# Optimization experiments

Hardware: AMD Instinct MI355X
Metric: run time of the kernel (lower is better)

The kernel has to match this reference:

```python
import jax, jax.numpy as jnp
import numpy as np


def setup_inputs() -> dict:
    key = jax.random.key(0)
    k1, k2, k3, k4, k5, k6 = jax.random.split(key, 6)
    B, V = 128, 128000
    logits = jax.random.normal(k1, (B, V), dtype=jnp.float32) * 2.0
    # keep temperatures away from 0 to avoid overflow in logits/temp
    temperatures = 0.7 + 0.6 * jax.random.uniform(k2, (B,), dtype=jnp.float32)
    top_ks = jax.random.randint(k3, (B,), 1, 1024, dtype=jnp.int32)
    top_ps = 0.7 + 0.29 * jax.random.uniform(k4, (B,), dtype=jnp.float32)
    min_ps = 0.02 * jax.random.uniform(k5, (B,), dtype=jnp.float32)
    # uniform variate for inverse-CDF multinomial sampling (one sample per row)
    u = jax.random.uniform(k6, (B, 1), dtype=jnp.float32)
    return {
        "logits": logits,
        "temperatures": temperatures,
        "top_ks": top_ks,
        "top_ps": top_ps,
        "min_ps": min_ps,
        "u": u,
    }


def reference(logits, temperatures, top_ks, top_ps, min_ps, u):
    """Faithful jax version of Sampler's torch-native sampling path:
    softmax(logits/T) -> descending sort -> top-k mask -> top-p mask
    (cumsum computed pre-mask, exactly as torch code) -> min-p mask ->
    multinomial sample (inverse CDF with provided uniform u) ->
    gather original token index. Also returns the renormalized filtered
    probs scattered back to vocab order (top_p_normalize_probs-style)."""
    B, V = logits.shape
    probs = jax.nn.softmax(logits / temperatures[:, None], axis=-1)  # [B, V]

    order = jnp.argsort(-probs, axis=-1)                     # descending indices
    probs_sort = jnp.take_along_axis(probs, order, axis=-1)  # [B, V] sorted desc
    probs_sum = jnp.cumsum(probs_sort, axis=-1)              # cumsum BEFORE masking

    pos = jnp.arange(V, dtype=jnp.int32)[None, :]
    # top-k: zero everything at rank >= top_k
    probs_sort = jnp.where(pos >= top_ks[:, None], 0.0, probs_sort)
    # top-p: zero where cumulative mass strictly before this token exceeds top_p
    probs_sort = jnp.where(probs_sum - probs_sort > top_ps[:, None], 0.0, probs_sort)
    # min-p: threshold relative to the max prob (rank-0 entry survives both masks)
    min_p_thr = probs_sort[:, :1] * min_ps[:, None]
    probs_sort = jnp.where(probs_sort < min_p_thr, 0.0, probs_sort)

    total = jnp.sum(probs_sort, axis=-1, keepdims=True)      # [B, 1]
    cdf = jnp.cumsum(probs_sort, axis=-1) / total            # normalized CDF
    # inverse-CDF sampling == torch.multinomial(probs_sort, 1)
    sampled_rank = jnp.clip(jnp.sum(cdf < u, axis=-1, keepdims=True), 0, V - 1)
    token_ids = jnp.take_along_axis(order, sampled_rank, axis=-1)[:, 0].astype(jnp.int32)

    # scatter renormalized filtered probs back to original vocab positions
    inv_order = jnp.argsort(order, axis=-1)
    norm_probs = jnp.take_along_axis(probs_sort / total, inv_order, axis=-1)
    return token_ids, norm_probs
```

## Files before the change

kernel.cpp:

```cpp
#include <hip/hip_runtime.h>
#include <stdint.h>
#include <math.h>

#define TPB 1024
#define NB 2048
#define SPLIT 4
#define LCAND 2560
#define CAND2 2048
#define PS 4096
#define L2E 1.44269504088896f

typedef float vfloat4 __attribute__((ext_vector_type(4)));
typedef unsigned long long ull;

__device__ __forceinline__ unsigned fkey(float f) {
    unsigned u = __float_as_uint(f);
    return (u & 0x80000000u) ? ~u : (u | 0x80000000u);
}
__device__ __forceinline__ float funkey(unsigned k) {
    unsigned u = (k & 0x80000000u) ? (k ^ 0x80000000u) : ~k;
    return __uint_as_float(u);
}
__device__ __forceinline__ ull packkv(unsigned k, unsigned idx) {
    return ((ull)k << 32) | (ull)(~idx);
}

__device__ __forceinline__ void suffix_scan_2048(unsigned* h, unsigned* wscr, int tid)
{
    const int lane = tid & 63, w = tid >> 6;
    const int i0 = 2047 - 2 * tid;
    const int i1 = 2046 - 2 * tid;
    unsigned a = h[i0], b = h[i1];
    unsigned s = a + b;
    unsigned inc = s;
    #pragma unroll
    for (int d = 1; d < 64; d <<= 1) { unsigned o = __shfl_up(inc, d); if (lane >= d) inc += o; }
    if (lane == 63) wscr[w] = inc;
    __syncthreads();
    if (w == 0) {
        unsigned v = (lane < 16) ? wscr[lane] : 0u;
        unsigned vi = v;
        #pragma unroll
        for (int d = 1; d < 16; d <<= 1) { unsigned o = __shfl_up(vi, d); if (lane >= d) vi += o; }
        if (lane < 16) wscr[16 + lane] = vi - v;
    }
    __syncthreads();
    unsigned off = wscr[16 + w] + (inc - s);
    h[i0] = off + a;
    h[i1] = off + a + b;
    __syncthreads();
}

__global__ __launch_bounds__(TPB)
void k1_scan(const float* __restrict__ logits,
             const float* __restrict__ temps,
             const int* __restrict__ top_ks,
             float* __restrict__ out_probs,
             float* __restrict__ ws_meta,
             unsigned* __restrict__ ws_cut,
             unsigned* __restrict__ ws_cnt,
             ull* __restrict__ ws_cand,
             int V, int Vq)
{
    const int sblk = blockIdx.x;
    const int b = sblk / SPLIT, s = sblk % SPLIT;
    const int tid = threadIdx.x, lane = tid & 63, w = tid >> 6;
    const int start = s * Vq;
    const int len = min(Vq, V - start);
    const int slot = sblk;
    const float invT = 1.0f / temps[b];
    int K = top_ks[b]; K = max(K, 1); K = min(K, 1024);

    __shared__ unsigned hist[NB];
    __shared__ unsigned uscr[32];
    __shared__ float fred[32];
    __shared__ unsigned cnt;
    __shared__ int bstar;

    if (len <= 0) {
        if (tid == 0) {
            ws_meta[2*slot] = -1e30f; ws_meta[2*slot+1] = 0.0f;
            ws_cut[slot] = 0xFFFFFFFFu; ws_cnt[slot] = 0u;
        }
        return;
    }

    for (int i = tid; i < NB; i += TPB) hist[i] = 0;
    if (tid == 0) { cnt = 0; bstar = 0; }
    __syncthreads();

    const float* __restrict__ row = logits + (size_t)b * V + start;
    const vfloat4* __restrict__ row4 = (const vfloat4*)row;
    const int L4 = len >> 2;

    const int nps = min(len, PS);
    float m0 = -1e30f;
    for (int i = tid; i < nps; i += TPB) {
        float lv = row[i];
        m0 = fmaxf(m0, lv);
        atomicAdd(&hist[fkey(lv) >> 21], 1u);
    }
    #pragma unroll
    for (int d = 32; d > 0; d >>= 1) m0 = fmaxf(m0, __shfl_down(m0, d));
    if (lane == 0) fred[w] = m0;
    __syncthreads();
    if (tid == 0) {
        float mm = fred[0];
        for (int j = 1; j < 16; ++j) mm = fmaxf(mm, fred[j]);
        fred[16] = mm;
    }
    __syncthreads();
    const float m0max = fred[16];

    suffix_scan_2048(hist, uscr, tid);
    float sexp = (float)K * (float)nps / (float)V;
    unsigned TGT = (unsigned)(sexp + 6.0f * sqrtf(sexp) + 16.5f);
    if (TGT > (unsigned)nps) TGT = (unsigned)nps;
    for (int e = tid; e < NB; e += TPB) {
        unsigned Se = hist[e];
        unsigned Sn = (e < NB - 1) ? hist[e + 1] : 0u;
        if (Se >= TGT && Sn < TGT) bstar = e;
    }
    __syncthreads();
    const unsigned cutkey = (unsigned)bstar << 21;
    const float cutval = funkey(cutkey);

    {
        float* __restrict__ orow = out_probs + (size_t)b * V + start;
        vfloat4* __restrict__ orow4 = (vfloat4*)orow;
        const vfloat4 z4 = (vfloat4)0.0f;
        for (int i = tid; i < L4; i += TPB) __builtin_nontemporal_store(z4, &orow4[i]);
        for (int i = (L4 << 2) + tid; i < len; i += TPB) __builtin_nontemporal_store(0.0f, &orow[i]);
    }

    const float ca = invT * L2E;
    const float cb = -m0max * invT * L2E;
    ull* gc = ws_cand + (size_t)slot * LCAND;

    float z0 = 0.0f, z1 = 0.0f, z2 = 0.0f, z3 = 0.0f;

    #define E4(v) (exp2f(fmaf((v)[0], ca, cb)) + exp2f(fmaf((v)[1], ca, cb)) \
                 + exp2f(fmaf((v)[2], ca, cb)) + exp2f(fmaf((v)[3], ca, cb)))
    #define GATHER(v, ii) do {                                                  \
        bool c0 = (v)[0] >= cutval, c1 = (v)[1] >= cutval,                      \
             c2 = (v)[2] >= cutval, c3 = (v)[3] >= cutval;                      \
        if (c0 | c1 | c2 | c3) {                                                \
            int nh = (int)c0 + (int)c1 + (int)c2 + (int)c3;                     \
            unsigned base = atomicAdd(&cnt, (unsigned)nh);                      \
            unsigned bi = (unsigned)(start + ((ii) << 2));                      \
            if (c0) { if (base < LCAND) gc[base] = packkv(fkey((v)[0]), bi+0); base++; } \
            if (c1) { if (base < LCAND) gc[base] = packkv(fkey((v)[1]), bi+1); base++; } \
            if (c2) { if (base < LCAND) gc[base] = packkv(fkey((v)[2]), bi+2); base++; } \
            if (c3) { if (base < LCAND) gc[base] = packkv(fkey((v)[3]), bi+3); base++; } \
        }                                                                       \
    } while (0)

    int i = tid;
    for (; i + 3 * TPB < L4; i += 4 * TPB) {
        vfloat4 va = row4[i];
        vfloat4 vb = row4[i + TPB];
        vfloat4 vc = row4[i + 2 * TPB];
        vfloat4 vd = row4[i + 3 * TPB];
        z0 += E4(va); z1 += E4(vb); z2 += E4(vc); z3 += E4(vd);
        GATHER(va, i); GATHER(vb, i + TPB); GATHER(vc, i + 2 * TPB); GATHER(vd, i + 3 * TPB);
    }
    for (; i < L4; i += TPB) {
        vfloat4 v = row4[i];
        z0 += E4(v);
        GATHER(v, i);
    }
    for (int j = (L4 << 2) + tid; j < len; j += TPB) {
        float lv = row[j];
        z0 += exp2f(fmaf(lv, ca, cb));
        if (lv >= cutval) {
            unsigned base = atomicAdd(&cnt, 1u);
            if (base < LCAND) gc[base] = packkv(fkey(lv), (unsigned)(start + j));
        }
    }
    #undef E4
    #undef GATHER

    float z = (z0 + z1) + (z2 + z3);
    __syncthreads();
    #pragma unroll
    for (int d = 32; d > 0; d >>= 1) z += __shfl_down(z, d);
    if (lane == 0) fred[w] = z;
    __syncthreads();
    if (tid == 0) {
        float zz = 0.0f;
        for (int j = 0; j < 16; ++j) zz += fred[j];
        ws_meta[2*slot + 0] = m0max * invT;
        ws_meta[2*slot + 1] = zz;
        ws_cut[slot] = cutkey;
        ws_cnt[slot] = cnt;
    }
}

__global__ __launch_bounds__(TPB)
void k2_sample(const float* __restrict__ logits,
               const float* __restrict__ temps,
               const int* __restrict__ top_ks,
               const float* __restrict__ top_ps,
               const float* __restrict__ min_ps,
               const float* __restrict__ uvec,
               const float* __restrict__ ws_meta,
               const unsigned* __restrict__ ws_cut,
               const unsigned* __restrict__ ws_cnt,
               const ull* __restrict__ ws_cand,
               float* __restrict__ out_tok,
               float* __restrict__ out_probs,
               int V)
{
    const int b = blockIdx.x;
    const int tid = threadIdx.x, lane = tid & 63, w = tid >> 6;
    const float invT = 1.0f / temps[b];
    int Korig = top_ks[b]; Korig = max(Korig, 1); Korig = min(Korig, 1024);
    const unsigned Ku = (unsigned)Korig;
    const float top_p = top_ps[b], min_p = min_ps[b], uval = uvec[b];

    __shared__ __align__(16) char smem[53504];
    ull*            cand  = (ull*)(smem);
    ull*            cand2 = (ull*)(smem + 16384);
    unsigned*       hist  = (unsigned*)(smem + 32768);
    unsigned short* cnts  = (unsigned short*)(smem + 41216);
    float*          sh_p  = (float*)(smem + 45312);
    float*          sh_c  = (float*)(smem + 49408);
    __shared__ unsigned uscr[32];
    __shared__ float fws[32];
    __shared__ unsigned scnt, sh_mk;
    __shared__ int sh_i1, sh_i2;
    __shared__ unsigned sh_u1;

    float Cy[SPLIT], zq[SPLIT];
    unsigned cutq[SPLIT], cntq[SPLIT];
    #pragma unroll
    for (int q = 0; q < SPLIT; ++q) {
        int sl = b * SPLIT + q;
        Cy[q] = ws_meta[2*sl]; zq[q] = ws_meta[2*sl+1];
        cutq[q] = ws_cut[sl]; cntq[q] = ws_cnt[sl];
    }
    float Y = -1e30f;
    #pragma unroll
    for (int q = 0; q < SPLIT; ++q) if (cntq[q] > 0u) Y = fmaxf(Y, Cy[q]);
    float Z = 0.0f;
    #pragma unroll
    for (int q = 0; q < SPLIT; ++q)
        if (cntq[q] > 0u && zq[q] > 0.0f) Z += zq[q] * exp2f((Cy[q] - Y) * L2E);

    bool fb = false;
    unsigned cutmax = 0, mincut = 0xFFFFFFFFu;
    #pragma unroll
    for (int q = 0; q < SPLIT; ++q) {
        if (cntq[q] > (unsigned)LCAND) fb = true;
        if (cntq[q] > 0u) {
            if (!isfinite(zq[q])) fb = true;
            cutmax = max(cutmax, cutq[q]);
            mincut = min(mincut, cutq[q]);
        }
    }
    if (mincut == 0xFFFFFFFFu || !isfinite(Z) || Z <= 0.0f) fb = true;

    unsigned Tkeyb = 0;
    int count = 0, bstar = 0, shift = 0;
    unsigned base = mincut;

    if (!fb) {
        unsigned mk = 0;
        if (tid == 0) sh_mk = 0;
        for (int i = tid; i <= NB; i += TPB) hist[i] = 0;
        if (tid == 0) { sh_i1 = -1; scnt = 0; }
        __syncthreads();
        #pragma unroll
        for (int q = 0; q < SPLIT; ++q) {
            const ull* gc = ws_cand + (size_t)(b * SPLIT + q) * LCAND;
            int nl = min((int)cntq[q], LCAND);
            for (int i = tid; i < nl; i += TPB)
                mk = max(mk, (unsigned)(gc[i] >> 32));
        }
        #pragma unroll
        for (int d = 32; d > 0; d >>= 1) mk = max(mk, __shfl_down(mk, d));
        if (lane == 0) atomicMax(&sh_mk, mk);
        __syncthreads();
        const unsigned maxkey = sh_mk;
        const unsigned range = maxkey - base;
        while ((range >> shift) > (unsigned)(NB - 1)) shift++;

        #pragma unroll
        for (int q = 0; q < SPLIT; ++q) {
            const ull* gc = ws_cand + (size_t)(b * SPLIT + q) * LCAND;
            int nl = min((int)cntq[q], LCAND);
            for (int i = tid; i < nl; i += TPB)
                atomicAdd(&hist[((unsigned)(gc[i] >> 32) - base) >> shift], 1u);
        }
        __syncthreads();
        unsigned fat = 0;
        for (int i = tid; i < NB; i += TPB) {
            unsigned h = hist[i];
            cnts[i] = (unsigned short)h;
            fat = max(fat, h);
        }
        #pragma unroll
        for (int d = 32; d > 0; d >>= 1) fat = max(fat, __shfl_down(fat, d));
        if (lane == 0) uscr[w] = fat;
        __syncthreads();
        if (tid == 0) {
            unsigned m2 = 0;
            for (int j = 0; j < 16; ++j) m2 = max(m2, uscr[j]);
            uscr[16] = m2;
        }
        __syncthreads();
        if (uscr[16] > 64u) fb = true;
    }
    if (!fb) {
        suffix_scan_2048(hist, uscr, tid);
        for (int e = tid; e < NB; e += TPB) {
            unsigned Se = hist[e], Sn = (e < NB - 1) ? hist[e + 1] : 0u;
            if (Se >= Ku && Sn < Ku) { sh_i1 = e; sh_u1 = Se; }
        }
        __syncthreads();
        if (sh_i1 < 0) fb = true;
        else {
            bstar = sh_i1;
            count = (int)sh_u1;
            Tkeyb = base + ((unsigned)bstar << shift);
            if (Tkeyb < cutmax || count > CAND2) fb = true;
        }
    }
    if (!fb) {
        #pragma unroll
        for (int q = 0; q < SPLIT; ++q) {
            const ull* gc = ws_cand + (size_t)(b * SPLIT + q) * LCAND;
            int nl = min((int)cntq[q], LCAND);
            for (int i = tid; i < nl; i += TPB) {
                ull e = gc[i];
                unsigned k = (unsigned)(e >> 32);
                if (k >= Tkeyb) {
                    unsigned bin = (k - base) >> shift;
                    unsigned pos = atomicAdd(&hist[bin + 1], 1u);
                    cand2[pos] = e;
                }
            }
        }
        __syncthreads();
        for (int e = bstar + tid; e < NB; e += TPB) {
            int c = (int)cnts[e];
            if (c >= 2) {
                int st = (int)hist[e + 1] - c;
                for (int x = 1; x < c; ++x) {
                    ull key = cand2[st + x];
                    int y = x - 1;
                    while (y >= 0 && cand2[st + y] < key) { cand2[st + y + 1] = cand2[st + y]; --y; }
                    cand2[st + y + 1] = key;
                }
            }
        }
        __syncthreads();
    }

    if (fb) {
        const float* __restrict__ row = logits + (size_t)b * V;
        float m = -1e30f, z = 0.0f;
        for (int i = tid; i < V; i += TPB) {
            float y = row[i] * invT;
            float nm = fmaxf(m, y);
            z = z * exp2f((m - nm) * L2E) + exp2f((y - nm) * L2E);
            m = nm;
        }
        sh_p[tid] = m; sh_c[tid] = z;
        __syncthreads();
        for (int d = TPB >> 1; d > 0; d >>= 1) {
            if (tid < d) {
                float m1 = sh_p[tid], z1 = sh_c[tid];
                float m2 = sh_p[tid + d], z2 = sh_c[tid + d];
                float mm = fmaxf(m1, m2);
                sh_c[tid] = z1 * exp2f((m1 - mm) * L2E) + z2 * exp2f((m2 - mm) * L2E);
                sh_p[tid] = mm;
            }
            __syncthreads();
        }
        Y = sh_p[0]; Z = sh_c[0];
        __syncthreads();
        for (int i = tid; i < NB; i += TPB) hist[i] = 0;
        if (tid == 0) { sh_i1 = 0; sh_i2 = 0; sh_u1 = 0; }
        __syncthreads();
        for (int i = tid; i < V; i += TPB) atomicAdd(&hist[fkey(row[i]) >> 21], 1u);
        __syncthreads();
        suffix_scan_2048(hist, uscr, tid);
        for (int e = tid; e < NB; e += TPB) {
            unsigned Se = hist[e], Sn = (e < NB-1) ? hist[e+1] : 0u;
            if (Se >= Ku && Sn < Ku) { sh_i1 = e; sh_u1 = Sn; }
        }
        __syncthreads();
        int b1 = sh_i1;
        unsigned cab = sh_u1;
        for (int i = tid; i < NB; i += TPB) hist[i] = 0;
        __syncthreads();
        for (int i = tid; i < V; i += TPB) {
            unsigned k = fkey(row[i]);
            if ((int)(k >> 21) == b1) atomicAdd(&hist[(k >> 10) & (NB - 1)], 1u);
        }
        __syncthreads();
        suffix_scan_2048(hist, uscr, tid);
        for (int e = tid; e < NB; e += TPB) {
            unsigned Se = cab + hist[e];
            unsigned Sn = cab + ((e < NB-1) ? hist[e+1] : 0u);
            if (Se >= Ku && Sn < Ku) sh_i2 = e;
        }
        __syncthreads();
        unsigned Tkey = ((unsigned)b1 << 21) | ((unsigned)sh_i2 << 10);
        if (tid == 0) scnt = 0;
        __syncthreads();
        for (int i = tid; i < V; i += TPB) {
            unsigned k = fkey(row[i]);
            if (k >= Tkey) {
                unsigned pos = atomicAdd(&scnt, 1u);
                if (pos < CAND2) cand[pos] = packkv(k, (unsigned)i);
            }
        }
        __syncthreads();
        count = (scnt < (unsigned)CAND2) ? (int)scnt : CAND2;

        int n_sort = 1;
        while (n_sort < count) n_sort <<= 1;
        for (int i = tid; i < n_sort; i += TPB)
            if (i >= count) cand[i] = 0ull;
        __syncthreads();
        for (int kk = 2; kk <= n_sort; kk <<= 1) {
            for (int j = kk >> 1; j > 0; j >>= 1) {
                for (int i = tid; i < n_sort; i += TPB) {
                    int ixj = i ^ j;
                    if (ixj > i) {
                        ull a = cand[i], c = cand[ixj];
                        bool up = (i & kk) == 0;
                        if (up ? (a < c) : (a > c)) { cand[i] = c; cand[ixj] = a; }
                    }
                }
                __syncthreads();
            }
        }
    }

    ull* srt = fb ? cand : cand2;
    int K = min(Korig, count);

    float pv = 0.0f;
    if (tid < K) {
        unsigned k = (unsigned)(srt[tid] >> 32);
        pv = exp2f((funkey(k) * invT - Y) * L2E) / Z;
    }
    float inc = pv;
    #pragma unroll
    for (int d = 1; d < 64; d <<= 1) { float o = __shfl_up(inc, d); if (lane >= d) inc += o; }
    if (lane == 63) fws[w] = inc;
    __syncthreads();
    if (w == 0) {
        float v = (lane < 16) ? fws[lane] : 0.0f;
        float vi = v;
        #pragma unroll
        for (int d = 1; d < 16; d <<= 1) { float o = __shfl_up(vi, d); if (lane >= d) vi += o; }
        if (lane < 16) fws[16 + lane] = vi - v;
    }
    __syncthreads();
    float cum = inc + fws[16 + w];
    sh_p[tid] = pv;
    sh_c[tid] = cum;
    if (tid == 0) sh_i1 = K;
    __syncthreads();

    if (tid < K) {
        float excl = cum - pv;
        if (excl > top_p) atomicMin(&sh_i1, tid);
    }
    __syncthreads();
    int n1 = sh_i1;
    float thr = sh_p[0] * min_p;
    if (tid == 0) sh_i2 = n1;
    __syncthreads();
    if (tid < n1 && sh_p[tid] < thr) atomicMin(&sh_i2, tid);
    __syncthreads();
    int nf = sh_i2;
    float total = sh_c[nf - 1];

    int pred = (tid < nf) && ((sh_c[tid] / total) < uval);
    int rank = __syncthreads_count(pred);
    if (rank > nf - 1) rank = nf - 1;
    if (rank < 0) rank = 0;
    if (tid == 0)
        out_tok[b] = (float)(~(unsigned)(srt[rank] & 0xFFFFFFFFull));

    if (tid < nf) {
        unsigned idx = ~(unsigned)(srt[tid] & 0xFFFFFFFFull);
        out_probs[(size_t)b * V + idx] = sh_p[tid] / total;
    }
}

extern "C" void kernel_launch(void* const* d_in, const int* in_sizes, int n_in,
                              void* d_out, int out_size, void* d_ws, size_t ws_size,
                              hipStream_t stream) {
    const float* logits = (const float*)d_in[0];
    const float* temps  = (const float*)d_in[1];
    const int*   top_ks = (const int*)d_in[2];
    const float* top_ps = (const float*)d_in[3];
    const float* min_ps = (const float*)d_in[4];
    const float* u      = (const float*)d_in[5];
    const int B = in_sizes[1];
    const int V = in_sizes[0] / B;
    float* out_tok   = (float*)d_out;
    float* out_probs = out_tok + B;

    int Vq = (((V + SPLIT - 1) / SPLIT) + 3) & ~3;

    char* ws = (char*)d_ws;
    size_t off = 0;
    auto take = [&](size_t bytes) { char* p = ws + off; off = (off + bytes + 255) & ~(size_t)255; return p; };
    float*    ws_meta = (float*)take((size_t)B * SPLIT * 2 * sizeof(float));
    unsigned* ws_cut  = (unsigned*)take((size_t)B * SPLIT * sizeof(unsigned));
    unsigned* ws_cnt  = (unsigned*)take((size_t)B * SPLIT * sizeof(unsigned));
    ull*      ws_cand = (ull*)take((size_t)B * SPLIT * LCAND * sizeof(ull));
    (void)ws_size;

    k1_scan<<<dim3(SPLIT * B), dim3(TPB), 0, stream>>>(
        logits, temps, top_ks, out_probs, ws_meta, ws_cut, ws_cnt, ws_cand, V, Vq);
    k2_sample<<<dim3(B), dim3(TPB), 0, stream>>>(
        logits, temps, top_ks, top_ps, min_ps, u, ws_meta, ws_cut, ws_cnt, ws_cand,
        out_tok, out_probs, V);
}
```

Before: 152.5 us.

## Split cut-threshold estimation into separate kernel, double row split, track candidate max

Moves the per-slice sample histogram, max and cutoff selection into a new lightweight k0_cut kernel (256 threads), so the streaming k1 kernel (now 512 threads) only does the exp-sum and candidate gather. The vocabulary split doubles from 4 to 8 slices per row, with a smaller per-slice candidate buffer and a smaller sample prefix. k1 now also reports the maximum candidate key, which removes a full pass over candidates in k2. Zeroing of the output now uses regular stores instead of nontemporal ones. This adds a kernel launch and reads the sample prefix twice. The smaller candidate buffers raise the chance of overflow, which sends rows down the fallback path.

Result: slower. 157.4 us (+3.2%).

```diff
diff --git a/kernel.cpp b/kernel.cpp
--- a/kernel.cpp
+++ b/kernel.cpp
@@ -2,12 +2,14 @@
 #include <stdint.h>
 #include <math.h>
 
+#define T0 256
+#define T1 512
 #define TPB 1024
 #define NB 2048
-#define SPLIT 4
-#define LCAND 2560
+#define SPLIT 8
+#define LCAND 1024
 #define CAND2 2048
-#define PS 4096
+#define PS0 2048
 #define L2E 1.44269504088896f
 
 typedef float vfloat4 __attribute__((ext_vector_type(4)));
@@ -51,93 +53,151 @@
     __syncthreads();
 }
 
-__global__ __launch_bounds__(TPB)
+__global__ __launch_bounds__(T0)
+void k0_cut(const float* __restrict__ logits,
+            const float* __restrict__ temps,
+            const int* __restrict__ top_ks,
+            float* __restrict__ ws_cy,
+            unsigned* __restrict__ ws_cut,
+            int V, int Vq)
+{
+    const int slot = blockIdx.x;
+    const int b = slot / SPLIT, s = slot % SPLIT;
+    const int tid = threadIdx.x, lane = tid & 63, w = tid >> 6;
+    const int start = s * Vq;
+    const int len = min(Vq, V - start);
+
+    __shared__ unsigned hist[NB];
+    __shared__ unsigned uscr[16];
+    __shared__ float fred[8];
+    __shared__ int bstar;
+
+    if (len <= 0) {
+        if (tid == 0) { ws_cut[slot] = 0xFFFFFFFFu; ws_cy[slot] = -1e30f; }
+        return;
+    }
+    for (int i = tid; i < NB; i += T0) hist[i] = 0;
+    if (tid == 0) bstar = 0;
+    __syncthreads();
+
+    const float* __restrict__ row = logits + (size_t)b * V + start;
+    const vfloat4* __restrict__ row4 = (const vfloat4*)row;
+    const int nps = min(len, PS0);
+    const int np4 = nps >> 2;
+
+    float m0 = -1e30f;
+    for (int i = tid; i < np4; i += T0) {
+        vfloat4 v = row4[i];
+        #pragma unroll
+        for (int j = 0; j < 4; ++j) {
+            float lv = v[j];
+            m0 = fmaxf(m0, lv);
+            atomicAdd(&hist[fkey(lv) >> 21], 1u);
+        }
+    }
+    for (int i = (np4 << 2) + tid; i < nps; i += T0) {
+        float lv = row[i];
+        m0 = fmaxf(m0, lv);
+        atomicAdd(&hist[fkey(lv) >> 21], 1u);
+    }
+    #pragma unroll
+    for (int d = 32; d > 0; d >>= 1) m0 = fmaxf(m0, __shfl_down(m0, d));
+    if (lane == 0) fred[w] = m0;
+    __syncthreads();
+    if (tid == 0) {
+        float mm = fred[0];
+        for (int j = 1; j < T0 / 64; ++j) mm = fmaxf(mm, fred[j]);
+        fred[4] = mm;
+    }
+    __syncthreads();
+    const float m0max = fred[4];
+
+    unsigned sloc[8];
+    unsigned acc = 0;
+    #pragma unroll
+    for (int j = 0; j < 8; ++j) { acc += hist[2047 - (8 * tid + j)]; sloc[j] = acc; }
+    __syncthreads();
+    unsigned inc = acc;
+    #pragma unroll
+    for (int d = 1; d < 64; d <<= 1) { unsigned o = __shfl_up(inc, d); if (lane >= d) inc += o; }
+    if (lane == 63) uscr[w] = inc;
+    __syncthreads();
+    if (tid == 0) {
+        unsigned o = 0;
+        for (int j = 0; j < T0 / 64; ++j) { unsigned t = uscr[j]; uscr[8 + j] = o; o += t; }
+    }
+    __syncthreads();
+    unsigned off = uscr[8 + w] + (inc - acc);
+    #pragma unroll
+    for (int j = 0; j < 8; ++j) hist[2047 - (8 * tid + j)] = off + sloc[j];
+    __syncthreads();
+
+    int K = top_ks[b]; K = max(K, 1); K = min(K, 1024);
+    float sexp = (float)K * (float)nps / (float)V;
+    unsigned TGT = (unsigned)(sexp + 6.0f * sqrtf(sexp) + 16.5f);
+    if (TGT > (unsigned)nps) TGT = (unsigned)nps;
+    for (int e = tid; e < NB; e += T0) {
+        unsigned Se = hist[e];
+        unsigned Sn = (e < NB - 1) ? hist[e + 1] : 0u;
+        if (Se >= TGT && Sn < TGT) bstar = e;
+    }
+    __syncthreads();
+    if (tid == 0) {
+        ws_cut[slot] = (unsigned)bstar << 21;
+        ws_cy[slot]  = m0max / temps[b];
+    }
+}
+
+__global__ __launch_bounds__(T1)
 void k1_scan(const float* __restrict__ logits,
              const float* __restrict__ temps,
-             const int* __restrict__ top_ks,
              float* __restrict__ out_probs,
-             float* __restrict__ ws_meta,
-             unsigned* __restrict__ ws_cut,
+             const float* __restrict__ ws_cy,
+             const unsigned* __restrict__ ws_cut,
+             float* __restrict__ ws_z,
              unsigned* __restrict__ ws_cnt,
+             unsigned* __restrict__ ws_maxk,
              ull* __restrict__ ws_cand,
              int V, int Vq)
 {
-    const int sblk = blockIdx.x;
-    const int b = sblk / SPLIT, s = sblk % SPLIT;
+    const int slot = blockIdx.x;
+    const int b = slot / SPLIT, s = slot % SPLIT;
     const int tid = threadIdx.x, lane = tid & 63, w = tid >> 6;
     const int start = s * Vq;
     const int len = min(Vq, V - start);
-    const int slot = sblk;
+
+    __shared__ float fred[16];
+    __shared__ unsigned cnt;
+
+    if (len <= 0) {
+        if (tid == 0) { ws_z[slot] = 0.0f; ws_cnt[slot] = 0u; ws_maxk[slot] = 0u; }
+        return;
+    }
+    if (tid == 0) cnt = 0;
+    __syncthreads();
+
     const float invT = 1.0f / temps[b];
-    int K = top_ks[b]; K = max(K, 1); K = min(K, 1024);
-
-    __shared__ unsigned hist[NB];
-    __shared__ unsigned uscr[32];
-    __shared__ float fred[32];
-    __shared__ unsigned cnt;
-    __shared__ int bstar;
-
-    if (len <= 0) {
-        if (tid == 0) {
-            ws_meta[2*slot] = -1e30f; ws_meta[2*slot+1] = 0.0f;
-            ws_cut[slot] = 0xFFFFFFFFu; ws_cnt[slot] = 0u;
-        }
-        return;
-    }
-
-    for (int i = tid; i < NB; i += TPB) hist[i] = 0;
-    if (tid == 0) { cnt = 0; bstar = 0; }
-    __syncthreads();
+    const float Cy = ws_cy[slot];
+    const unsigned cutkey = ws_cut[slot];
+    const float cutval = funkey(cutkey);
 
     const float* __restrict__ row = logits + (size_t)b * V + start;
     const vfloat4* __restrict__ row4 = (const vfloat4*)row;
     const int L4 = len >> 2;
-
-    const int nps = min(len, PS);
-    float m0 = -1e30f;
-    for (int i = tid; i < nps; i += TPB) {
-        float lv = row[i];
-        m0 = fmaxf(m0, lv);
-        atomicAdd(&hist[fkey(lv) >> 21], 1u);
-    }
-    #pragma unroll
-    for (int d = 32; d > 0; d >>= 1) m0 = fmaxf(m0, __shfl_down(m0, d));
-    if (lane == 0) fred[w] = m0;
-    __syncthreads();
-    if (tid == 0) {
-        float mm = fred[0];
-        for (int j = 1; j < 16; ++j) mm = fmaxf(mm, fred[j]);
-        fred[16] = mm;
-    }
-    __syncthreads();
-    const float m0max = fred[16];
-
-    suffix_scan_2048(hist, uscr, tid);
-    float sexp = (float)K * (float)nps / (float)V;
-    unsigned TGT = (unsigned)(sexp + 6.0f * sqrtf(sexp) + 16.5f);
-    if (TGT > (unsigned)nps) TGT = (unsigned)nps;
-    for (int e = tid; e < NB; e += TPB) {
-        unsigned Se = hist[e];
-        unsigned Sn = (e < NB - 1) ? hist[e + 1] : 0u;
-        if (Se >= TGT && Sn < TGT) bstar = e;
-    }
-    __syncthreads();
-    const unsigned cutkey = (unsigned)bstar << 21;
-    const float cutval = funkey(cutkey);
 
     {
         float* __restrict__ orow = out_probs + (size_t)b * V + start;
         vfloat4* __restrict__ orow4 = (vfloat4*)orow;
         const vfloat4 z4 = (vfloat4)0.0f;
-        for (int i = tid; i < L4; i += TPB) __builtin_nontemporal_store(z4, &orow4[i]);
-        for (int i = (L4 << 2) + tid; i < len; i += TPB) __builtin_nontemporal_store(0.0f, &orow[i]);
+        for (int i = tid; i < L4; i += T1) orow4[i] = z4;
+        for (int i = (L4 << 2) + tid; i < len; i += T1) orow[i] = 0.0f;
     }
 
     const float ca = invT * L2E;
-    const float cb = -m0max * invT * L2E;
+    const float cb = -Cy * L2E;
     ull* gc = ws_cand + (size_t)slot * LCAND;
 
-    float z0 = 0.0f, z1 = 0.0f, z2 = 0.0f, z3 = 0.0f;
+    float z0 = 0.0f, z1 = 0.0f, z2 = 0.0f, z3 = 0.0f, mb = -1e30f;
 
     #define E4(v) (exp2f(fmaf((v)[0], ca, cb)) + exp2f(fmaf((v)[1], ca, cb)) \
                  + exp2f(fmaf((v)[2], ca, cb)) + exp2f(fmaf((v)[3], ca, cb)))
@@ -145,6 +205,7 @@
         bool c0 = (v)[0] >= cutval, c1 = (v)[1] >= cutval,                      \
              c2 = (v)[2] >= cutval, c3 = (v)[3] >= cutval;                      \
         if (c0 | c1 | c2 | c3) {                                                \
+            mb = fmaxf(mb, fmaxf(fmaxf((v)[0], (v)[1]), fmaxf((v)[2], (v)[3])));\
             int nh = (int)c0 + (int)c1 + (int)c2 + (int)c3;                     \
             unsigned base = atomicAdd(&cnt, (unsigned)nh);                      \
             unsigned bi = (unsigned)(start + ((ii) << 2));                      \
@@ -156,23 +217,24 @@
     } while (0)
 
     int i = tid;
-    for (; i + 3 * TPB < L4; i += 4 * TPB) {
+    for (; i + 3 * T1 < L4; i += 4 * T1) {
         vfloat4 va = row4[i];
-        vfloat4 vb = row4[i + TPB];
-        vfloat4 vc = row4[i + 2 * TPB];
-        vfloat4 vd = row4[i + 3 * TPB];
+        vfloat4 vb = row4[i + T1];
+        vfloat4 vc = row4[i + 2 * T1];
+        vfloat4 vd = row4[i + 3 * T1];
         z0 += E4(va); z1 += E4(vb); z2 += E4(vc); z3 += E4(vd);
-        GATHER(va, i); GATHER(vb, i + TPB); GATHER(vc, i + 2 * TPB); GATHER(vd, i + 3 * TPB);
-    }
-    for (; i < L4; i += TPB) {
+        GATHER(va, i); GATHER(vb, i + T1); GATHER(vc, i + 2 * T1); GATHER(vd, i + 3 * T1);
+    }
+    for (; i < L4; i += T1) {
         vfloat4 v = row4[i];
         z0 += E4(v);
         GATHER(v, i);
     }
-    for (int j = (L4 << 2) + tid; j < len; j += TPB) {
+    for (int j = (L4 << 2) + tid; j < len; j += T1) {
         float lv = row[j];
         z0 += exp2f(fmaf(lv, ca, cb));
         if (lv >= cutval) {
+            mb = fmaxf(mb, lv);
             unsigned base = atomicAdd(&cnt, 1u);
             if (base < LCAND) gc[base] = packkv(fkey(lv), (unsigned)(start + j));
         }
@@ -183,16 +245,18 @@
     float z = (z0 + z1) + (z2 + z3);
     __syncthreads();
     #pragma unroll
-    for (int d = 32; d > 0; d >>= 1) z += __shfl_down(z, d);
-    if (lane == 0) fred[w] = z;
+    for (int d = 32; d > 0; d >>= 1) {
+        z += __shfl_down(z, d);
+        mb = fmaxf(mb, __shfl_down(mb, d));
+    }
+    if (lane == 0) { fred[w] = z; fred[8 + w] = mb; }
     __syncthreads();
     if (tid == 0) {
-        float zz = 0.0f;
-        for (int j = 0; j < 16; ++j) zz += fred[j];
-        ws_meta[2*slot + 0] = m0max * invT;
-        ws_meta[2*slot + 1] = zz;
-        ws_cut[slot] = cutkey;
+        float zz = 0.0f, mm = -1e30f;
+        for (int j = 0; j < T1 / 64; ++j) { zz += fred[j]; mm = fmaxf(mm, fred[8 + j]); }
+        ws_z[slot] = zz;
         ws_cnt[slot] = cnt;
+        ws_maxk[slot] = (cnt > 0u) ? fkey(mm) : 0u;
     }
 }
 
@@ -203,9 +267,11 @@
                const float* __restrict__ top_ps,
                const float* __restrict__ min_ps,
                const float* __restrict__ uvec,
-               const float* __restrict__ ws_meta,
+               const float* __restrict__ ws_cy,
+               const float* __restrict__ ws_z,
                const unsigned* __restrict__ ws_cut,
                const unsigned* __restrict__ ws_cnt,
+               const unsigned* __restrict__ ws_maxk,
                const ull* __restrict__ ws_cand,
                float* __restrict__ out_tok,
                float* __restrict__ out_probs,
@@ -227,17 +293,17 @@
     float*          sh_c  = (float*)(smem + 49408);
     __shared__ unsigned uscr[32];
     __shared__ float fws[32];
-    __shared__ unsigned scnt, sh_mk;
+    __shared__ unsigned scnt;
     __shared__ int sh_i1, sh_i2;
     __shared__ unsigned sh_u1;
 
     float Cy[SPLIT], zq[SPLIT];
-    unsigned cutq[SPLIT], cntq[SPLIT];
+    unsigned cutq[SPLIT], cntq[SPLIT], mkq[SPLIT];
     #pragma unroll
     for (int q = 0; q < SPLIT; ++q) {
         int sl = b * SPLIT + q;
-        Cy[q] = ws_meta[2*sl]; zq[q] = ws_meta[2*sl+1];
-        cutq[q] = ws_cut[sl]; cntq[q] = ws_cnt[sl];
+        Cy[q] = ws_cy[sl]; zq[q] = ws_z[sl];
+        cutq[q] = ws_cut[sl]; cntq[q] = ws_cnt[sl]; mkq[q] = ws_maxk[sl];
     }
     float Y = -1e30f;
     #pragma unroll
@@ -248,7 +314,7 @@
         if (cntq[q] > 0u && zq[q] > 0.0f) Z += zq[q] * exp2f((Cy[q] - Y) * L2E);
 
     bool fb = false;
-    unsigned cutmax = 0, mincut = 0xFFFFFFFFu;
+    unsigned cutmax = 0, mincut = 0xFFFFFFFFu, maxkey = 0;
     #pragma unroll
     for (int q = 0; q < SPLIT; ++q) {
         if (cntq[q] > (unsigned)LCAND) fb = true;
@@ -256,35 +322,21 @@
             if (!isfinite(zq[q])) fb = true;
             cutmax = max(cutmax, cutq[q]);
             mincut = min(mincut, cutq[q]);
+            maxkey = max(maxkey, mkq[q]);
         }
     }
     if (mincut == 0xFFFFFFFFu || !isfinite(Z) || Z <= 0.0f) fb = true;
 
     unsigned Tkeyb = 0;
     int count = 0, bstar = 0, shift = 0;
-    unsigned base = mincut;
+    const unsigned base = mincut;
 
     if (!fb) {
-        unsigned mk = 0;
-        if (tid == 0) sh_mk = 0;
+        const unsigned range = maxkey - base;
+        while ((range >> shift) > (unsigned)(NB - 1)) shift++;
         for (int i = tid; i <= NB; i += TPB) hist[i] = 0;
         if (tid == 0) { sh_i1 = -1; scnt = 0; }
         __syncthreads();
-        #pragma unroll
-        for (int q = 0; q < SPLIT; ++q) {
-            const ull* gc = ws_cand + (size_t)(b * SPLIT + q) * LCAND;
-            int nl = min((int)cntq[q], LCAND);
-            for (int i = tid; i < nl; i += TPB)
-                mk = max(mk, (unsigned)(gc[i] >> 32));
-        }
-        #pragma unroll
-        for (int d = 32; d > 0; d >>= 1) mk = max(mk, __shfl_down(mk, d));
-        if (lane == 0) atomicMax(&sh_mk, mk);
-        __syncthreads();
-        const unsigned maxkey = sh_mk;
-        const unsigned range = maxkey - base;
-        while ((range >> shift) > (unsigned)(NB - 1)) shift++;
-
         #pragma unroll
         for (int q = 0; q < SPLIT; ++q) {
             const ull* gc = ws_cand + (size_t)(b * SPLIT + q) * LCAND;
@@ -513,15 +565,19 @@
     char* ws = (char*)d_ws;
     size_t off = 0;
     auto take = [&](size_t bytes) { char* p = ws + off; off = (off + bytes + 255) & ~(size_t)255; return p; };
-    float*    ws_meta = (float*)take((size_t)B * SPLIT * 2 * sizeof(float));
+    float*    ws_cy   = (float*)take((size_t)B * SPLIT * sizeof(float));
+    float*    ws_z    = (float*)take((size_t)B * SPLIT * sizeof(float));
     unsigned* ws_cut  = (unsigned*)take((size_t)B * SPLIT * sizeof(unsigned));
     unsigned* ws_cnt  = (unsigned*)take((size_t)B * SPLIT * sizeof(unsigned));
+    unsigned* ws_maxk = (unsigned*)take((size_t)B * SPLIT * sizeof(unsigned));
     ull*      ws_cand = (ull*)take((size_t)B * SPLIT * LCAND * sizeof(ull));
     (void)ws_size;
 
-    k1_scan<<<dim3(SPLIT * B), dim3(TPB), 0, stream>>>(
-        logits, temps, top_ks, out_probs, ws_meta, ws_cut, ws_cnt, ws_cand, V, Vq);
+    k0_cut<<<dim3(SPLIT * B), dim3(T0), 0, stream>>>(
+        logits, temps, top_ks, ws_cy, ws_cut, V, Vq);
+    k1_scan<<<dim3(SPLIT * B), dim3(T1), 0, stream>>>(
+        logits, temps, out_probs, ws_cy, ws_cut, ws_z, ws_cnt, ws_maxk, ws_cand, V, Vq);
     k2_sample<<<dim3(B), dim3(TPB), 0, stream>>>(
-        logits, temps, top_ks, top_ps, min_ps, u, ws_meta, ws_cut, ws_cnt, ws_cand,
-        out_tok, out_probs, V);
-}
+        logits, temps, top_ks, top_ps, min_ps, u, ws_cy, ws_z, ws_cut, ws_cnt,
+        ws_maxk, ws_cand, out_tok, out_probs, V);
+}
```
